# Kernel tuning notes

Measured on AMD Instinct MI355X. Metric: run time of the kernel, lower is better.

## Reference

```python
import jax, jax.numpy as jnp
import numpy as np

B, C, H, W = 2, 64, 128, 128
K, SCALE, NUM_RES = 3, 2, 2
KK = K * K


def conv(x, w, b, pad=0):
    y = jax.lax.conv_general_dilated(x, w, (1, 1), [(pad, pad), (pad, pad)],
                                     dimension_numbers=('NCHW', 'OIHW', 'NCHW'))
    return y + b[None, :, None, None]


def unfold_dilated(x, k, d):
    # mimics nn.Unfold(kernel_size=k, dilation=d, padding=(k//2)*d) -> (b, c, k*k, h, w)
    pad = (k // 2) * d
    b, c, h, w = x.shape
    xp = jnp.pad(x, ((0, 0), (0, 0), (pad, pad), (pad, pad)))
    slices = [xp[:, :, i * d:i * d + h, j * d:j * d + w]
              for i in range(k) for j in range(k)]
    return jnp.stack(slices, axis=2)


def setup_inputs() -> dict:
    key = jax.random.key(0)
    ks = jax.random.split(key, 32)
    def p(k, shape, s=0.05):
        return jax.random.normal(k, shape, dtype=jnp.float32) * s
    H2, W2 = H * SCALE, W * SCALE
    return {
        'depth':  p(ks[0], (B, C, H2, W2), 1.0),
        'guide':  p(ks[1], (B, C, H2, W2), 1.0),
        'inputs': p(ks[2], (B, C, H, W), 1.0),
        # depth_kernel branch: 1x1 C->C (ReLU), 1x1 C->k^2
        'dk_w1': p(ks[3], (C, C, 1, 1)), 'dk_b1': jnp.zeros((C,), jnp.float32),
        'dk_w2': p(ks[4], (KK, C, 1, 1)), 'dk_b2': jnp.zeros((KK,), jnp.float32),
        # guide_kernel branch
        'gk_w1': p(ks[5], (C, C, 1, 1)), 'gk_b1': jnp.zeros((C,), jnp.float32),
        'gk_w2': p(ks[6], (KK, C, 1, 1)), 'gk_b2': jnp.zeros((KK,), jnp.float32),
        # weight_net: 3x3 2C->C (ReLU), 3x3 C->C (ReLU, TUnet stand-in), 3x3 C->1
        'wn_w1': p(ks[7], (C, 2 * C, 3, 3)), 'wn_b1': jnp.zeros((C,), jnp.float32),
        'wn_w2': p(ks[8], (C, C, 3, 3)), 'wn_b2': jnp.zeros((C,), jnp.float32),
        'wn_w3': p(ks[9], (1, C, 3, 3)), 'wn_b3': jnp.zeros((1,), jnp.float32),
        # residual blocks on inputs: NUM_RES x (conv3x3-ReLU-conv3x3 + skip)
        'rb_w': p(ks[10], (NUM_RES, 2, C, C, 3, 3)),
        'rb_b': jnp.zeros((NUM_RES, 2, C), jnp.float32),
        'aff_scale': 0.5 * KK * jnp.ones((1,), jnp.float32),
    }


def reference(depth, guide, inputs,
              dk_w1, dk_b1, dk_w2, dk_b2,
              gk_w1, gk_b1, gk_w2, gk_b2,
              wn_w1, wn_b1, wn_w2, wn_b2, wn_w3, wn_b3,
              rb_w, rb_b, aff_scale):
    # weight map
    wm = jax.nn.relu(conv(jnp.concatenate([depth, guide], axis=1), wn_w1, wn_b1, 1))
    wm = jax.nn.relu(conv(wm, wn_w2, wn_b2, 1))
    weight_map = conv(wm, wn_w3, wn_b3, 1)                       # (b,1,h_,w_)
    # per-pixel kernels
    dk = conv(jax.nn.relu(conv(depth, dk_w1, dk_b1)), dk_w2, dk_b2)
    gk = conv(jax.nn.relu(conv(guide, gk_w1, gk_b1)), gk_w2, gk_b2)
    dk = jax.nn.softmax(dk, axis=1)
    gk = jax.nn.softmax(gk, axis=1)
    fuse = weight_map * dk + (1.0 - weight_map) * gk
    fuse = jnp.tanh(fuse) / (aff_scale + 1e-8)
    ksum = jnp.maximum(jnp.sum(jnp.abs(fuse), axis=1, keepdims=True) + 1e-4, 1.0)
    fuse = fuse / ksum                                            # (b,k^2,h_,w_)
    # residual conv stack on low-res inputs
    x = inputs
    for i in range(NUM_RES):
        r = jax.nn.relu(conv(x, rb_w[i, 0], rb_b[i, 0], 1))
        r = conv(r, rb_w[i, 1], rb_b[i, 1], 1)
        x = x + r
    b, c, h, w = x.shape
    up = jax.image.resize(x, (b, c, h * SCALE, w * SCALE), method='bilinear')
    unf = unfold_dilated(up, K, SCALE)                            # (b,c,k^2,h_,w_)
    out = jnp.einsum('bkhw,bckhw->bchw', fuse, unf)
    return out
```

## Files before the change

### kernel.cpp

```cpp
#include <hip/hip_runtime.h>
#include <hip/hip_bf16.h>
#include <math.h>
#include <stdint.h>

#define HW2 (256*256)
#define HW1 (128*128)

typedef __attribute__((ext_vector_type(8))) short short8;
typedef __attribute__((ext_vector_type(4))) float floatx4;

__device__ __forceinline__ float b2f(ushort u) {
    union { unsigned int i; float f; } v; v.i = ((unsigned int)u) << 16; return v.f;
}
__device__ __forceinline__ ushort f2b(float f) {
    __hip_bfloat16 h = __float2bfloat16(f); return *(ushort*)&h;
}
__device__ __forceinline__ float fast_tanh(float x) {
    float cx = fminf(fmaxf(x, -15.f), 15.f);
    float t = __expf(2.f * cx);
    return (t - 1.f) / (t + 1.f);
}
__device__ __forceinline__ void gload_lds16(const void* g, void* l) {
    __builtin_amdgcn_global_load_lds(
        (__attribute__((address_space(1))) void*)(uintptr_t)g,
        (__attribute__((address_space(3))) void*)(unsigned)(uintptr_t)l,
        16, 0, 0);
}


__device__ __forceinline__
void repack_body(int gx, int role, int tid,
                 const float* __restrict__ wn_w1, const float* __restrict__ wn_w2,
                 const float* __restrict__ rb_w,
                 const float* __restrict__ dk_w1, const float* __restrict__ gk_w1,
                 const float* __restrict__ dk_w2, const float* __restrict__ gk_w2,
                 const float* __restrict__ wn_w3,
                 ushort* __restrict__ wt_wn1, ushort* __restrict__ wt_wn2,
                 ushort* __restrict__ wt_rb,
                 ushort* __restrict__ w1d, ushort* __restrict__ w1g,
                 ushort* __restrict__ w2d, ushort* __restrict__ w2g,
                 ushort* __restrict__ wt3) {
    int idx = gx * 256 + tid;
    if (role == 0) {
        if (idx >= 73728) return;
        int o = idx / 1152; int rem = idx - o * 1152;
        int ci = rem / 9;   int t = rem - ci * 9;
        wt_wn1[(((size_t)(ci >> 5) * 9 + t) * 64 + o) * 32 + (ci & 31)] = f2b(wn_w1[idx]);
    } else if (role <= 5) {
        if (idx >= 36864) return;
        const float* w = (role == 1) ? wn_w2 : rb_w + (size_t)(role - 2) * 36864;
        ushort* wt     = (role == 1) ? wt_wn2 : wt_rb + (size_t)(role - 2) * 36864;
        int o = idx / 576; int rem = idx - o * 576;
        int ci = rem / 9;  int t = rem - ci * 9;
        wt[(((size_t)(ci >> 5) * 9 + t) * 64 + o) * 32 + (ci & 31)] = f2b(w[idx]);
    } else if (role == 6) {
        if (idx >= 10240) return;
        if (idx < 4096)      w1d[idx] = f2b(dk_w1[idx]);
        else if (idx < 8192) w1g[idx - 4096] = f2b(gk_w1[idx - 4096]);
        else if (idx < 9216) { int i = idx - 8192; w2d[i] = (i >> 6) < 9 ? f2b(dk_w2[i]) : (ushort)0; }
        else                 { int i = idx - 9216; w2g[i] = (i >> 6) < 9 ? f2b(gk_w2[i]) : (ushort)0; }
    } else {
        if (idx >= 9216) return;
        int kc = idx / 512; int rem = idx - kc * 512;
        int n = rem >> 5, c = rem & 31;
        int cc = kc / 9, t = kc - cc * 9;
        wt3[idx] = (n == 0) ? f2b(wn_w3[(cc * 32 + c) * 9 + t]) : (ushort)0;
    }
}

__device__ __forceinline__
void to_chunked_body(int gx, int bc, int tid,
                     const float* __restrict__ in, ushort* __restrict__ outc,
                     int H, int W, int Cchunks) {
    int P = W + 2, Q = H + 2;
    int plane_px = P * Q;
    int idx = gx * 256 + tid;
    if (idx >= plane_px) return;
    int py = idx / P, px = idx - py * P;
    int b = bc / Cchunks, cc = bc - b * Cchunks;
    ushort* dst = outc + ((size_t)bc * plane_px + idx) * 32;
    short8* d8 = (short8*)dst;
    if (py == 0 || py == Q - 1 || px == 0 || px == P - 1) {
        short8 z = (short8){0, 0, 0, 0, 0, 0, 0, 0};
        d8[0] = z; d8[1] = z; d8[2] = z; d8[3] = z;
        return;
    }
    int y = py - 1, x = px - 1;
    const float* src = in + ((size_t)b * (Cchunks * 32) + cc * 32) * H * W
                          + (size_t)y * W + x;
    ushort tmp[32];
#pragma unroll
    for (int c = 0; c < 32; ++c)
        tmp[c] = f2b(src[(size_t)c * H * W]);
#pragma unroll
    for (int v = 0; v < 4; ++v) d8[v] = *(short8*)&tmp[v * 8];
}

__device__ __forceinline__
void hi4_body(int bx, int tid,
              const float* __restrict__ depth, const float* __restrict__ guide,
              ushort* __restrict__ outc) {
    int gid = bx * 256 + tid;
    int g   = gid & 63;
    int y   = (gid >> 6) & 255;
    int pl  = gid >> 14;
    const float* srcb = (pl < 4) ? depth : guide;
    int bc = pl & 3;
    int b = bc >> 1, cc = bc & 1;
    const float* src = srcb + ((size_t)b * 64 + cc * 32) * HW2 + (size_t)y * 256 + g * 4;
    ushort tmp[4][32];
#pragma unroll
    for (int c = 0; c < 32; ++c) {
        floatx4 v = *(const floatx4*)&src[(size_t)c * HW2];
        tmp[0][c] = f2b(v[0]); tmp[1][c] = f2b(v[1]);
        tmp[2][c] = f2b(v[2]); tmp[3][c] = f2b(v[3]);
    }
    ushort* dst = outc + ((size_t)pl * 258 * 258 + (size_t)(y + 1) * 258 + (g * 4 + 1)) * 32;
#pragma unroll
    for (int p = 0; p < 4; ++p) {
        short8* d8 = (short8*)(dst + (size_t)p * 32);
        d8[0] = *(short8*)&tmp[p][0];
        d8[1] = *(short8*)&tmp[p][8];
        d8[2] = *(short8*)&tmp[p][16];
        d8[3] = *(short8*)&tmp[p][24];
    }
}

__device__ __forceinline__
void zero_body(int gx, int region, int tid,
               ushort* __restrict__ buf256, ushort* __restrict__ buf128,
               ushort* __restrict__ bufhi) {
    int H = (region == 1) ? 128 : 256;
    int P = H + 2, Q = H + 2;
    ushort* buf = (region == 0) ? buf256 : (region == 1) ? buf128 : bufhi;
    int nb = 2 * P + 2 * H;
    int idx = gx * 256 + tid;
    if (idx >= nb * 8) return;
    int pl = idx / nb, r = idx - pl * nb;
    int py, px;
    if (r < P)          { py = 0;     px = r; }
    else if (r < 2 * P) { py = Q - 1; px = r - P; }
    else { int k = r - 2 * P; py = 1 + (k >> 1); px = (k & 1) ? P - 1 : 0; }
    ushort* dst = buf + ((size_t)pl * P * Q + (size_t)py * P + px) * 32;
    short8 z = (short8){0, 0, 0, 0, 0, 0, 0, 0};
    short8* d8 = (short8*)dst;
    d8[0] = z; d8[1] = z; d8[2] = z; d8[3] = z;
}

template<int NCHUNK, int ROWS, bool RELU, bool HAS_SKIP, bool CONCAT2>
__device__ __forceinline__
void conv_body(const ushort* __restrict__ inA, const ushort* __restrict__ inB,
               const ushort* __restrict__ wt, const float* __restrict__ bias,
               const ushort* __restrict__ skip, ushort* __restrict__ outc,
               int H, int W, int b, int bx, int by, int tid) {
    const int P = W + 2;
    const size_t plane = (size_t)P * (H + 2) * 32;
    int wv = tid >> 6, lane = tid & 63, ml = lane & 15, q = lane >> 4;
    int x0 = bx * 16;
    int yb = by * (4 * ROWS) + wv * ROWS;

    floatx4 acc[ROWS][4];
#pragma unroll
    for (int r = 0; r < ROWS; ++r)
#pragma unroll
        for (int n = 0; n < 4; ++n) acc[r][n] = (floatx4){0.f, 0.f, 0.f, 0.f};

    for (int cc = 0; cc < NCHUNK; ++cc) {
        const ushort* base;
        if (CONCAT2) {
            constexpr int HC = NCHUNK / 2;
            if (cc < HC) base = inA + ((size_t)(b * HC + cc)) * plane;
            else         base = inB + ((size_t)(b * HC + cc - HC)) * plane;
        } else {
            base = inA + ((size_t)(b * NCHUNK + cc)) * plane;
        }
        const ushort* wb = wt + (size_t)cc * 18432;
#pragma unroll
        for (int dy = 0; dy < 3; ++dy) {
            short8 afr[3][ROWS], bfr[3][4];
#pragma unroll
            for (int dx = 0; dx < 3; ++dx) {
#pragma unroll
                for (int r = 0; r < ROWS; ++r)
                    afr[dx][r] = *(const short8*)&base[((size_t)(yb + r + dy) * P
                                                       + (x0 + ml + dx)) * 32 + q * 8];
#pragma unroll
                for (int n = 0; n < 4; ++n)
                    bfr[dx][n] = *(const short8*)&wb[(size_t)((dy * 3 + dx) * 64
                                                              + n * 16 + ml) * 32 + q * 8];
            }
#pragma unroll
            for (int dx = 0; dx < 3; ++dx)
#pragma unroll
                for (int r = 0; r < ROWS; ++r)
#pragma unroll
                    for (int n = 0; n < 4; ++n)
                        acc[r][n] = __builtin_amdgcn_mfma_f32_16x16x32_bf16(
                            afr[dx][r], bfr[dx][n], acc[r][n], 0, 0, 0);
        }
    }

#pragma unroll
    for (int r = 0; r < ROWS; ++r) {
        int y = yb + r;
#pragma unroll
        for (int n = 0; n < 4; ++n) {
            int ch = n * 16 + ml;
            int occ = ch >> 5, ocl = ch & 31;
            float bs = bias[ch];
            size_t pbase = ((size_t)(b * 2 + occ)) * plane + ((size_t)(y + 1) * P) * 32 + ocl;
#pragma unroll
            for (int e = 0; e < 4; ++e) {
                int x = x0 + q * 4 + e;
                float v = acc[r][n][e] + bs;
                if (RELU) v = fmaxf(v, 0.f);
                if (HAS_SKIP)
                    v += b2f(skip[((size_t)(b * 2 + occ)) * plane
                                  + ((size_t)(y + 1) * P + (x + 1)) * 32 + ocl]);
                outc[pbase + (size_t)(x + 1) * 32] = f2b(v);
            }
        }
    }
}

__global__ __launch_bounds__(256)
void prep_all(const float* __restrict__ depth, const float* __restrict__ guide,
              const float* __restrict__ inputs,
              const float* __restrict__ wn_w1, const float* __restrict__ wn_w2,
              const float* __restrict__ rb_w,
              const float* __restrict__ dk_w1, const float* __restrict__ gk_w1,
              const float* __restrict__ dk_w2, const float* __restrict__ gk_w2,
              const float* __restrict__ wn_w3,
              ushort* __restrict__ depth_c, ushort* __restrict__ inp_c,
              ushort* __restrict__ wt_wn1, ushort* __restrict__ wt_wn2,
              ushort* __restrict__ wt_rb,
              ushort* __restrict__ w1d, ushort* __restrict__ w1g,
              ushort* __restrict__ w2d, ushort* __restrict__ w2g,
              ushort* __restrict__ wt3,
              ushort* __restrict__ bufA, ushort* __restrict__ r0) {
    int bx = blockIdx.x, tid = threadIdx.x;
    if (bx < 512) {
        hi4_body(bx, tid, depth, guide, depth_c);
    } else if (bx < 780) {
        int v = bx - 512;
        to_chunked_body(v % 67, v / 67, tid, inputs, inp_c, 128, 128, 2);
    } else if (bx < 3084) {
        int v = bx - 780;
        repack_body(v % 288, v / 288, tid, wn_w1, wn_w2, rb_w, dk_w1, gk_w1,
                    dk_w2, gk_w2, wn_w3, wt_wn1, wt_wn2, wt_rb,
                    w1d, w1g, w2d, w2g, wt3);
    } else {
        int v = bx - 3084;
        zero_body(v % 33, v / 33, tid, bufA, r0, depth_c);
    }
}

__global__ __launch_bounds__(256, 2)
void conv_pairA(const ushort* __restrict__ depth_c, const ushort* __restrict__ guide_c,
                const ushort* __restrict__ wt_wn1, const float* __restrict__ wn_b1,
                ushort* __restrict__ bufA,
                const ushort* __restrict__ inp_c, const ushort* __restrict__ wt_rb0,
                const float* __restrict__ rb_b0, ushort* __restrict__ r0) {
    int tid = threadIdx.x;
    if (blockIdx.z == 0) {
        int idx = blockIdx.y * 16 + blockIdx.x;
        int b = idx >> 7, rem = idx & 127;
        conv_body<2, 2, true, false, false>(inp_c, nullptr, wt_rb0, rb_b0, nullptr,
                                            r0, 128, 128, b, rem & 7, rem >> 3, tid);
    } else {
        conv_body<4, 4, true, false, true>(depth_c, guide_c, wt_wn1, wn_b1, nullptr,
                                           bufA, 256, 256, blockIdx.z - 1,
                                           blockIdx.x, blockIdx.y, tid);
    }
}

__global__ __launch_bounds__(256, 2)
void conv_pairB(const ushort* __restrict__ bufA,
                const ushort* __restrict__ wt_wn2, const float* __restrict__ wn_b2,
                ushort* __restrict__ bufB,
                const ushort* __restrict__ r0, const ushort* __restrict__ wt_rb1,
                const float* __restrict__ rb_b1, const ushort* __restrict__ inp_c,
                ushort* __restrict__ r1) {
    int tid = threadIdx.x;
    if (blockIdx.z == 0) {
        int idx = blockIdx.y * 16 + blockIdx.x;
        int b = idx >> 7, rem = idx & 127;
        conv_body<2, 2, false, true, false>(r0, nullptr, wt_rb1, rb_b1, inp_c,
                                            r1, 128, 128, b, rem & 7, rem >> 3, tid);
    } else {
        conv_body<2, 4, true, false, false>(bufA, nullptr, wt_wn2, wn_b2, nullptr,
                                            bufB, 256, 256, blockIdx.z - 1,
                                            blockIdx.x, blockIdx.y, tid);
    }
}

__global__ __launch_bounds__(256, 2)
void fuse_rb2(const ushort* __restrict__ depth_c, const ushort* __restrict__ guide_c,
              const ushort* __restrict__ bufB,
              const ushort* __restrict__ wt3, const float* __restrict__ wn_b3,
              const ushort* __restrict__ w1d, const float* __restrict__ b1d,
              const ushort* __restrict__ w2d, const float* __restrict__ b2d,
              const ushort* __restrict__ w1g, const float* __restrict__ b1g,
              const ushort* __restrict__ w2g, const float* __restrict__ b2g,
              const float* __restrict__ aff, float* __restrict__ fuse_out,
              const ushort* __restrict__ r1, const ushort* __restrict__ wt_rb2,
              const float* __restrict__ rb_b2, ushort* __restrict__ r0) {
    int tid = threadIdx.x;
    if (blockIdx.x < 256) {
        int idx = blockIdx.x;
        int b = idx >> 7, rem = idx & 127;
        conv_body<2, 2, true, false, false>(r1, nullptr, wt_rb2, rb_b2, nullptr,
                                            r0, 128, 128, b, rem & 7, rem >> 3, tid);
        return;
    }
    int bxl = blockIdx.x - 256;

    __shared__ __align__(16) ushort stage[12672];
    __shared__ __align__(16) ushort hid[2][4][16 * 72];
    __shared__ float wmv[4][16];

    int wv = tid >> 6, lane = tid & 63, ml = lane & 15, q = lane >> 4;
    int p0 = bxl * 64 + wv * 16;
    int b = p0 >> 16, rem0 = p0 & 65535;
    const size_t plane = (size_t)258 * 258 * 32;

    int rem = rem0 + ml;
    int y = rem >> 8, x = rem & 255;
    size_t poff = ((size_t)(y + 1) * 258 + (x + 1)) * 32;

    int pb  = bxl * 64;
    int y0  = (pb & 65535) >> 8;
    int x0b = pb & 255;

    short8 afr[2][2];
#pragma unroll
    for (int kc = 0; kc < 2; ++kc) {
        afr[0][kc] = *(const short8*)&depth_c[(size_t)(b * 2 + kc) * plane + poff + q * 8];
        afr[1][kc] = *(const short8*)&guide_c[(size_t)(b * 2 + kc) * plane + poff + q * 8];
    }

    const ushort* bbase = bufB + (size_t)(b * 2) * plane;
#pragma unroll
    for (int i = 0; i < 7; ++i) {
        int wofs = i * 4096 + (wv << 10);
        int ofs  = wofs + (lane << 4);
        if (ofs < 25344) {
            int seg = ofs / 4224;
            int within = ofs - seg * 4224;
            int cc2 = seg / 3, r = seg - cc2 * 3;
            const ushort* gsrc = bbase + (size_t)cc2 * plane
                               + ((size_t)(y0 + r) * 258 + x0b) * 32 + (within >> 1);
            gload_lds16(gsrc, (char*)stage + wofs);
        }
    }
    __syncthreads();

    floatx4 acc[2][4];
#pragma unroll
    for (int br = 0; br < 2; ++br)
#pragma unroll
        for (int nt = 0; nt < 4; ++nt) acc[br][nt] = (floatx4){0.f, 0.f, 0.f, 0.f};
#pragma unroll
    for (int nt = 0; nt < 4; ++nt)
#pragma unroll
        for (int kc = 0; kc < 2; ++kc) {
            short8 bD = *(const short8*)&w1d[(size_t)((nt * 16 + ml) * 64 + kc * 32 + q * 8)];
            short8 bG = *(const short8*)&w1g[(size_t)((nt * 16 + ml) * 64 + kc * 32 + q * 8)];
            acc[0][nt] = __builtin_amdgcn_mfma_f32_16x16x32_bf16(afr[0][kc], bD, acc[0][nt], 0, 0, 0);
            acc[1][nt] = __builtin_amdgcn_mfma_f32_16x16x32_bf16(afr[1][kc], bG, acc[1][nt], 0, 0, 0);
        }

    int colb = (wv << 4) + ml;
    floatx4 dw[4];
#pragma unroll
    for (int u = 0; u < 4; ++u) dw[u] = (floatx4){0.f, 0.f, 0.f, 0.f};
#pragma unroll
    for (int t = 0; t < 9; ++t) {
        int dy2 = t / 3, dx2 = t - 3 * dy2;
        short8 a0 = *(const short8*)&stage[(size_t)(dy2 * 66 + colb + dx2) * 32 + q * 8];
        short8 b3 = *(const short8*)&wt3[(size_t)(t * 512 + ml * 32 + q * 8)];
        dw[t & 3] = __builtin_amdgcn_mfma_f32_16x16x32_bf16(a0, b3, dw[t & 3], 0, 0, 0);
    }
#pragma unroll
    for (int t = 0; t < 9; ++t) {
        int dy2 = t / 3, dx2 = t - 3 * dy2;
        short8 a1 = *(const short8*)&stage[(size_t)((3 + dy2) * 66 + colb + dx2) * 32 + q * 8];
        short8 b3 = *(const short8*)&wt3[(size_t)((9 + t) * 512 + ml * 32 + q * 8)];
        dw[t & 3] = __builtin_amdgcn_mfma_f32_16x16x32_bf16(a1, b3, dw[t & 3], 0, 0, 0);
    }
    floatx4 dwm = (dw[0] + dw[1]) + (dw[2] + dw[3]);
    if (ml == 0) {
#pragma unroll
        for (int e = 0; e < 4; ++e) wmv[wv][q * 4 + e] = dwm[e];
    }

#pragma unroll
    for (int br = 0; br < 2; ++br) {
        const float* b1 = br ? b1g : b1d;
        ushort* h = hid[br][wv];
#pragma unroll
        for (int nt = 0; nt < 4; ++nt) {
            float bs = b1[nt * 16 + ml];
#pragma unroll
            for (int e = 0; e < 4; ++e) {
                float v = acc[br][nt][e] + bs;
                v = fmaxf(v, 0.f);
                h[(q * 4 + e) * 72 + nt * 16 + ml] = f2b(v);
            }
        }
    }

    floatx4 d2[2];
    d2[0] = (floatx4){0.f, 0.f, 0.f, 0.f};
    d2[1] = (floatx4){0.f, 0.f, 0.f, 0.f};
#pragma unroll
    for (int kc = 0; kc < 2; ++kc) {
        short8 a2d = *(const short8*)&w2d[(size_t)(ml * 64 + kc * 32 + q * 8)];
        short8 a2g = *(const short8*)&w2g[(size_t)(ml * 64 + kc * 32 + q * 8)];
        short8 hfd = *(const short8*)&hid[0][wv][ml * 72 + kc * 32 + q * 8];
        short8 hfg = *(const short8*)&hid[1][wv][ml * 72 + kc * 32 + q * 8];
        d2[0] = __builtin_amdgcn_mfma_f32_16x16x32_bf16(a2d, hfd, d2[0], 0, 0, 0);
        d2[1] = __builtin_amdgcn_mfma_f32_16x16x32_bf16(a2g, hfg, d2[1], 0, 0, 0);
    }

    float wm = wmv[wv][ml] + wn_b3[0];

    float sm[2][4];
#pragma unroll
    for (int br = 0; br < 2; ++br) {
        const float* b2 = br ? b2g : b2d;
        float lg[4];
#pragma unroll
        for (int e = 0; e < 4; ++e) {
            int j = q * 4 + e;
            lg[e] = (j < 9) ? (d2[br][e] + b2[j]) : -1e30f;
        }
        float m = fmaxf(fmaxf(lg[0], lg[1]), fmaxf(lg[2], lg[3]));
        m = fmaxf(m, __shfl_xor(m, 16));
        m = fmaxf(m, __shfl_xor(m, 32));
        float s = 0.f;
#pragma unroll
        for (int e = 0; e < 4; ++e) { lg[e] = __expf(lg[e] - m); s += lg[e]; }
        s += __shfl_xor(s, 16);
        s += __shfl_xor(s, 32);
        float inv = 1.f / s;
#pragma unroll
        for (int e = 0; e < 4; ++e) sm[br][e] = lg[e] * inv;
    }

    float inv_av = 1.f / (aff[0] + 1e-8f);
    float f[4];
    float s = 0.f;
#pragma unroll
    for (int e = 0; e < 4; ++e) {
        float v = wm * sm[0][e] + (1.f - wm) * sm[1][e];
        v = fast_tanh(v) * inv_av;
        f[e] = v;
        s += fabsf(v);
    }
    s += __shfl_xor(s, 16);
    s += __shfl_xor(s, 32);
    float ksum = s + 1e-4f;
    if (ksum < 1.f) ksum = 1.f;
    float invk = 1.f / ksum;
#pragma unroll
    for (int e = 0; e < 4; ++e) {
        int j = q * 4 + e;
        if (j < 9)
            fuse_out[((size_t)b * 9 + j) * HW2 + rem0 + ml] = f[e] * invk;
    }
}

__global__ __launch_bounds__(256, 2)
void conv_single(const ushort* __restrict__ inA, const ushort* __restrict__ wt,
                 const float* __restrict__ bias, const ushort* __restrict__ skip,
                 ushort* __restrict__ outc) {
    conv_body<2, 2, false, true, false>(inA, nullptr, wt, bias, skip, outc,
                                        128, 128, blockIdx.z,
                                        blockIdx.x, blockIdx.y, threadIdx.x);
}

__global__ __launch_bounds__(256)
void fuse_apply_up(const float* __restrict__ fuse, const ushort* __restrict__ r2c,
                   float* __restrict__ out) {
    int p = blockIdx.x * 256 + threadIdx.x;
    int b = blockIdx.y;
    int y = p >> 8, x = p & 255;

    int my = y >> 1, mx = x >> 1;
    float wyA = (y & 1) ? 0.75f : 0.25f;  float wyB = 1.f - wyA;
    float wxA = (x & 1) ? 0.75f : 0.25f;  float wxB = 1.f - wxA;
    int R0y = my + ((y & 1) ? 0 : -1) - 1;
    int R0x = mx + ((x & 1) ? 0 : -1) - 1;

    const float* f = fuse + (size_t)b * 9 * HW2 + p;
    float coef[4][4];
#pragma unroll
    for (int k = 0; k < 4; ++k)
#pragma unroll
        for (int l = 0; l < 4; ++l) coef[k][l] = 0.f;

#pragma unroll
    for (int ty = 0; ty < 3; ++ty) {
        int yp = y + (ty - 1) * 2;
        if (yp < 0 || yp > 255) continue;
#pragma unroll
        for (int tx = 0; tx < 3; ++tx) {
            int xp = x + (tx - 1) * 2;
            if (xp < 0 || xp > 255) continue;
            float fv = f[(size_t)(ty * 3 + tx) * HW2];
            coef[ty][tx]         += fv * wyA * wxA;
            coef[ty][tx + 1]     += fv * wyA * wxB;
            coef[ty + 1][tx]     += fv * wyB * wxA;
            coef[ty + 1][tx + 1] += fv * wyB * wxB;
        }
    }

    int ryv[4], rxv[4];
#pragma unroll
    for (int k = 0; k < 4; ++k) {
        int ry = R0y + k; ryv[k] = ry < 0 ? 0 : (ry > 127 ? 127 : ry);
        int rx = R0x + k; rxv[k] = rx < 0 ? 0 : (rx > 127 ? 127 : rx);
    }

    for (int cc = 0; cc < 2; ++cc) {
        const ushort* base = r2c + (size_t)(b * 2 + cc) * 130 * 130 * 32;
        float acc[32];
#pragma unroll
        for (int c = 0; c < 32; ++c) acc[c] = 0.f;
#pragma unroll
        for (int k = 0; k < 4; ++k) {
#pragma unroll
            for (int l = 0; l < 4; ++l) {
                float cf = coef[k][l];
                const ushort* u = base + ((size_t)(ryv[k] + 1) * 130 + (rxv[l] + 1)) * 32;
#pragma unroll
                for (int c = 0; c < 32; ++c) acc[c] = fmaf(cf, b2f(u[c]), acc[c]);
            }
        }
        float* ob = out + ((size_t)(b * 64 + cc * 32)) * HW2 + p;
#pragma unroll
        for (int c = 0; c < 32; ++c) ob[(size_t)c * HW2] = acc[c];
    }
}

extern "C" void kernel_launch(void* const* d_in, const int* in_sizes, int n_in,
                              void* d_out, int out_size, void* d_ws, size_t ws_size,
                              hipStream_t stream) {
    const float* depth  = (const float*)d_in[0];
    const float* guide  = (const float*)d_in[1];
    const float* inputs = (const float*)d_in[2];
    const float* dk_w1  = (const float*)d_in[3];
    const float* dk_b1  = (const float*)d_in[4];
    const float* dk_w2  = (const float*)d_in[5];
    const float* dk_b2  = (const float*)d_in[6];
    const float* gk_w1  = (const float*)d_in[7];
    const float* gk_b1  = (const float*)d_in[8];
    const float* gk_w2  = (const float*)d_in[9];
    const float* gk_b2  = (const float*)d_in[10];
    const float* wn_w1  = (const float*)d_in[11];
    const float* wn_b1  = (const float*)d_in[12];
    const float* wn_w2  = (const float*)d_in[13];
    const float* wn_b2  = (const float*)d_in[14];
    const float* wn_w3  = (const float*)d_in[15];
    const float* wn_b3  = (const float*)d_in[16];
    const float* rb_w   = (const float*)d_in[17];
    const float* rb_b   = (const float*)d_in[18];
    const float* aff    = (const float*)d_in[19];
    float* out = (float*)d_out;

    float* ws = (float*)d_ws;
    size_t off = 0;
    const size_t CH256 = 4260096;
    const size_t CH128 = 1081600;
    ushort* depth_c = (ushort*)(ws + off); off += CH256;
    ushort* guide_c = (ushort*)(ws + off); off += CH256;
    ushort* bufA    = (ushort*)(ws + off); off += CH256;
    ushort* bufB    = (ushort*)(ws + off); off += CH256;
    ushort* inp_c   = (ushort*)(ws + off); off += CH128;
    ushort* r0      = (ushort*)(ws + off); off += CH128;
    ushort* r1      = (ushort*)(ws + off); off += CH128;
    ushort* r2      = (ushort*)(ws + off); off += CH128;
    float* fuse     = ws + off; off += 1179648;
    ushort* wt_wn1  = (ushort*)(ws + off); off += 36864;
    ushort* wt_wn2  = (ushort*)(ws + off); off += 18432;
    ushort* wt_rb   = (ushort*)(ws + off); off += 73728;
    ushort* w1d_b   = (ushort*)(ws + off); off += 2048;
    ushort* w1g_b   = (ushort*)(ws + off); off += 2048;
    ushort* w2d_b   = (ushort*)(ws + off); off += 512;
    ushort* w2g_b   = (ushort*)(ws + off); off += 512;
    ushort* wt3_b   = (ushort*)(ws + off); off += 4608;

    prep_all<<<3183, 256, 0, stream>>>(
        depth, guide, inputs, wn_w1, wn_w2, rb_w, dk_w1, gk_w1, dk_w2, gk_w2,
        wn_w3, depth_c, inp_c, wt_wn1, wt_wn2, wt_rb,
        w1d_b, w1g_b, w2d_b, w2g_b, wt3_b, bufA, r0);

    conv_pairA<<<dim3(16, 16, 3), 256, 0, stream>>>(
        depth_c, guide_c, wt_wn1, wn_b1, bufA,
        inp_c, wt_rb + 0 * 36864, rb_b + 0 * 64, r0);

    conv_pairB<<<dim3(16, 16, 3), 256, 0, stream>>>(
        bufA, wt_wn2, wn_b2, bufB,
        r0, wt_rb + 1 * 36864, rb_b + 1 * 64, inp_c, r1);

    fuse_rb2<<<2304, 256, 0, stream>>>(
        depth_c, guide_c, bufB, wt3_b, wn_b3,
        w1d_b, dk_b1, w2d_b, dk_b2, w1g_b, gk_b1, w2g_b, gk_b2,
        aff, fuse,
        r1, wt_rb + 2 * 36864, rb_b + 2 * 64, r0);

    conv_single<<<dim3(8, 16, 2), 256, 0, stream>>>(
        r0, wt_rb + 3 * 36864, rb_b + 3 * 64, r1, r2);

    fuse_apply_up<<<dim3(256, 2), 256, 0, stream>>>(fuse, r2, out);
}
```

Baseline: 298.5 us.

## Split fuse kernel in halves to overlap both final residual convs; stage wt3 in LDS

```diff
diff --git a/kernel.cpp b/kernel.cpp
--- a/kernel.cpp
+++ b/kernel.cpp
@@ -294,28 +294,34 @@
     }
 }
 
+template<int HALF>
 __global__ __launch_bounds__(256, 2)
-void fuse_rb2(const ushort* __restrict__ depth_c, const ushort* __restrict__ guide_c,
-              const ushort* __restrict__ bufB,
-              const ushort* __restrict__ wt3, const float* __restrict__ wn_b3,
-              const ushort* __restrict__ w1d, const float* __restrict__ b1d,
-              const ushort* __restrict__ w2d, const float* __restrict__ b2d,
-              const ushort* __restrict__ w1g, const float* __restrict__ b1g,
-              const ushort* __restrict__ w2g, const float* __restrict__ b2g,
-              const float* __restrict__ aff, float* __restrict__ fuse_out,
-              const ushort* __restrict__ r1, const ushort* __restrict__ wt_rb2,
-              const float* __restrict__ rb_b2, ushort* __restrict__ r0) {
+void fuse_rb(const ushort* __restrict__ depth_c, const ushort* __restrict__ guide_c,
+             const ushort* __restrict__ bufB,
+             const ushort* __restrict__ wt3, const float* __restrict__ wn_b3,
+             const ushort* __restrict__ w1d, const float* __restrict__ b1d,
+             const ushort* __restrict__ w2d, const float* __restrict__ b2d,
+             const ushort* __restrict__ w1g, const float* __restrict__ b1g,
+             const ushort* __restrict__ w2g, const float* __restrict__ b2g,
+             const float* __restrict__ aff, float* __restrict__ fuse_out,
+             const ushort* __restrict__ rb_in, const ushort* __restrict__ rb_wt,
+             const float* __restrict__ rb_bias, const ushort* __restrict__ rb_skip,
+             ushort* __restrict__ rb_out) {
     int tid = threadIdx.x;
     if (blockIdx.x < 256) {
         int idx = blockIdx.x;
         int b = idx >> 7, rem = idx & 127;
-        conv_body<2, 2, true, false, false>(r1, nullptr, wt_rb2, rb_b2, nullptr,
-                                            r0, 128, 128, b, rem & 7, rem >> 3, tid);
+        if (HALF == 0)
+            conv_body<2, 2, true, false, false>(rb_in, nullptr, rb_wt, rb_bias, nullptr,
+                                                rb_out, 128, 128, b, rem & 7, rem >> 3, tid);
+        else
+            conv_body<2, 2, false, true, false>(rb_in, nullptr, rb_wt, rb_bias, rb_skip,
+                                                rb_out, 128, 128, b, rem & 7, rem >> 3, tid);
         return;
     }
-    int bxl = blockIdx.x - 256;
-
-    __shared__ __align__(16) ushort stage[12672];
+    int bxl = (blockIdx.x - 256) + HALF * 1024;
+
+    __shared__ __align__(16) ushort stage[21888];
     __shared__ __align__(16) ushort hid[2][4][16 * 72];
     __shared__ float wmv[4][16];
 
@@ -341,7 +347,7 @@
 
     const ushort* bbase = bufB + (size_t)(b * 2) * plane;
 #pragma unroll
-    for (int i = 0; i < 7; ++i) {
+    for (int i = 0; i < 11; ++i) {
         int wofs = i * 4096 + (wv << 10);
         int ofs  = wofs + (lane << 4);
         if (ofs < 25344) {
@@ -351,6 +357,9 @@
             const ushort* gsrc = bbase + (size_t)cc2 * plane
                                + ((size_t)(y0 + r) * 258 + x0b) * 32 + (within >> 1);
             gload_lds16(gsrc, (char*)stage + wofs);
+        } else if (ofs < 43776) {
+            const ushort* gsrc = wt3 + ((ofs - 25344) >> 1);
+            gload_lds16(gsrc, (char*)stage + wofs);
         }
     }
     __syncthreads();
@@ -371,6 +380,7 @@
         }
 
     int colb = (wv << 4) + ml;
+    const ushort* wt3l = stage + 12672;
     floatx4 dw[4];
 #pragma unroll
     for (int u = 0; u < 4; ++u) dw[u] = (floatx4){0.f, 0.f, 0.f, 0.f};
@@ -378,14 +388,14 @@
     for (int t = 0; t < 9; ++t) {
         int dy2 = t / 3, dx2 = t - 3 * dy2;
         short8 a0 = *(const short8*)&stage[(size_t)(dy2 * 66 + colb + dx2) * 32 + q * 8];
-        short8 b3 = *(const short8*)&wt3[(size_t)(t * 512 + ml * 32 + q * 8)];
+        short8 b3 = *(const short8*)&wt3l[(size_t)(t * 512 + ml * 32 + q * 8)];
         dw[t & 3] = __builtin_amdgcn_mfma_f32_16x16x32_bf16(a0, b3, dw[t & 3], 0, 0, 0);
     }
 #pragma unroll
     for (int t = 0; t < 9; ++t) {
         int dy2 = t / 3, dx2 = t - 3 * dy2;
         short8 a1 = *(const short8*)&stage[(size_t)((3 + dy2) * 66 + colb + dx2) * 32 + q * 8];
-        short8 b3 = *(const short8*)&wt3[(size_t)((9 + t) * 512 + ml * 32 + q * 8)];
+        short8 b3 = *(const short8*)&wt3l[(size_t)((9 + t) * 512 + ml * 32 + q * 8)];
         dw[t & 3] = __builtin_amdgcn_mfma_f32_16x16x32_bf16(a1, b3, dw[t & 3], 0, 0, 0);
     }
     floatx4 dwm = (dw[0] + dw[1]) + (dw[2] + dw[3]);
@@ -469,15 +479,6 @@
         if (j < 9)
             fuse_out[((size_t)b * 9 + j) * HW2 + rem0 + ml] = f[e] * invk;
     }
-}
-
-__global__ __launch_bounds__(256, 2)
-void conv_single(const ushort* __restrict__ inA, const ushort* __restrict__ wt,
-                 const float* __restrict__ bias, const ushort* __restrict__ skip,
-                 ushort* __restrict__ outc) {
-    conv_body<2, 2, false, true, false>(inA, nullptr, wt, bias, skip, outc,
-                                        128, 128, blockIdx.z,
-                                        blockIdx.x, blockIdx.y, threadIdx.x);
 }
 
 __global__ __launch_bounds__(256)
@@ -604,13 +605,16 @@
         bufA, wt_wn2, wn_b2, bufB,
         r0, wt_rb + 1 * 36864, rb_b + 1 * 64, inp_c, r1);
 
-    fuse_rb2<<<2304, 256, 0, stream>>>(
+    fuse_rb<0><<<1280, 256, 0, stream>>>(
         depth_c, guide_c, bufB, wt3_b, wn_b3,
         w1d_b, dk_b1, w2d_b, dk_b2, w1g_b, gk_b1, w2g_b, gk_b2,
         aff, fuse,
-        r1, wt_rb + 2 * 36864, rb_b + 2 * 64, r0);
-
-    conv_single<<<dim3(8, 16, 2), 256, 0, stream>>>(
+        r1, wt_rb + 2 * 36864, rb_b + 2 * 64, nullptr, r0);
+
+    fuse_rb<1><<<1280, 256, 0, stream>>>(
+        depth_c, guide_c, bufB, wt3_b, wn_b3,
+        w1d_b, dk_b1, w2d_b, dk_b2, w1g_b, gk_b1, w2g_b, gk_b2,
+        aff, fuse,
         r0, wt_rb + 3 * 36864, rb_b + 3 * 64, r1, r2);
 
     fuse_apply_up<<<dim3(256, 2), 256, 0, stream>>>(fuse, r2, out);
```

New measurement: 308.3 us. +3.3%, slower.
